# Optimization experiments

Measured on AMD Instinct MI355X. Metric: run time of the kernel, lower is better.

## Reference

```python
import jax, jax.numpy as jnp
import numpy as np

B, L = 2048, 64          # sentence pairs, leaves per balanced binary tree
V, IN, M, HID, NC = 50000, 300, 150, 50, 5


def setup_inputs() -> dict:
    key = jax.random.key(0)
    ks = jax.random.split(key, 16)
    lin = lambda k, fi, fo: jax.random.normal(k, (fi, fo), jnp.float32) / np.sqrt(fi).astype(np.float32)
    bias = lambda k, fo: jax.random.normal(k, (fo,), jnp.float32) * 0.01
    return {
        "ltokens": jax.random.randint(ks[0], (B, L), 0, V, dtype=jnp.int32),
        "rtokens": jax.random.randint(ks[1], (B, L), 0, V, dtype=jnp.int32),
        "emb":   jax.random.normal(ks[2], (V, IN), jnp.float32),
        "Wioux": lin(ks[3], IN, 3 * M), "bioux": bias(ks[4], 3 * M),
        "Wiouh": lin(ks[5], M, 3 * M), "biouh": bias(ks[6], 3 * M),
        "Wfx":   lin(ks[7], IN, M),    "bfx":   bias(ks[8], M),
        "Wfh":   lin(ks[9], M, M),     "bfh":   bias(ks[10], M),
        "Wh":    lin(ks[11], 2 * M, HID), "bh": bias(ks[12], HID),
        "Wp":    lin(ks[13], HID, NC),    "bp": bias(ks[14], NC),
    }


def _split_iou(iou, m):
    return iou[..., :m], iou[..., m:2 * m], iou[..., 2 * m:]


def _encode(tokens, emb, Wioux, bioux, Wiouh, biouh, Wfh, bfh):
    m = Wfh.shape[0]
    x = emb[tokens]                                   # [B, L, IN]
    # Leaves: child_h = child_c = 0, so iouh contributes only its bias and fc = 0.
    iou = x @ Wioux + bioux + biouh                   # [B, L, 3M]
    i, o, u = _split_iou(iou, m)
    c = jax.nn.sigmoid(i) * jnp.tanh(u)
    h = jax.nn.sigmoid(o) * jnp.tanh(c)
    # Internal nodes level by level (inputs=None branch of node_forward).
    while h.shape[1] > 1:
        Bq, n, _ = h.shape
        ch = h.reshape(Bq, n // 2, 2, m)              # children h
        cc = c.reshape(Bq, n // 2, 2, m)              # children c
        iou = ch.sum(axis=2) @ Wiouh + biouh          # child-sum
        i, o, u = _split_iou(iou, m)
        f = jax.nn.sigmoid(ch @ Wfh + bfh)            # per-child forget gate
        c = jax.nn.sigmoid(i) * jnp.tanh(u) + (f * cc).sum(axis=2)
        h = jax.nn.sigmoid(o) * jnp.tanh(c)
    # ROOT in the original just passes its single child's state through.
    return h[:, 0]                                    # [B, M]


def reference(ltokens, rtokens, emb, Wioux, bioux, Wiouh, biouh, Wfx, bfx, Wfh, bfh, Wh, bh, Wp, bp):
    lh = _encode(ltokens, emb, Wioux, bioux, Wiouh, biouh, Wfh, bfh)
    rh = _encode(rtokens, emb, Wioux, bioux, Wiouh, biouh, Wfh, bfh)
    vec = jnp.concatenate([lh * rh, jnp.abs(lh - rh)], axis=-1)   # [B, 2M]
    mid = jax.nn.sigmoid(vec @ Wh + bh)
    return jax.nn.log_softmax(mid @ Wp + bp, axis=-1)             # [B, NC]
```

## Files before the change

### kernel.cpp

```cpp
#include <hip/hip_runtime.h>
#include <hip/hip_bf16.h>
#include <math.h>

constexpr int B_   = 2048;
constexpr int L_   = 64;
constexpr int V_   = 50000;
constexpr int IN_  = 300;
constexpr int M_   = 150;
constexpr int HID_ = 50;
constexpr int NC_  = 5;

constexpr int KP_  = 160;
constexpr int GN_  = 608;
constexpr int GNT_ = 19;
constexpr int GKC_ = 5;
constexpr int GCH_ = GN_ * 32;
constexpr int GQS_ = GN_ * 8;
constexpr int LEAF_N  = 480;
constexpr int LEAF_NT = 15;
constexpr int LEAF_KC = 10;
constexpr int LEAF_CH = LEAF_N * 32;
constexpr int LEAF_QS = LEAF_N * 8;

typedef float f32x4  __attribute__((ext_vector_type(4)));
typedef short bf16x8 __attribute__((ext_vector_type(8)));
typedef short short4v __attribute__((ext_vector_type(4)));

__device__ __forceinline__ float rcp_f(float x) { return __builtin_amdgcn_rcpf(x); }
__device__ __forceinline__ float sgm(float x)   { return rcp_f(1.0f + __expf(-x)); }
__device__ __forceinline__ float tanh_f(float x){ return 1.0f - 2.0f * rcp_f(1.0f + __expf(2.0f * x)); }

__device__ __forceinline__ short f2bs(float f) {
    union { __hip_bfloat16 h; short s; } u; u.h = __float2bfloat16(f); return u.s;
}
__device__ __forceinline__ float bs2f(short s) {
    union { short s; __hip_bfloat16 h; } u; u.s = s; return __bfloat162float(u.h);
}

__device__ __forceinline__ void gl_lds16(const short* g, short* l) {
    __builtin_amdgcn_global_load_lds(
        (const __attribute__((address_space(1))) unsigned int*)g,
        (__attribute__((address_space(3))) unsigned int*)l, 16, 0, 0);
}

__global__ __launch_bounds__(256) void prep_kernel(
    const float* __restrict__ Wioux, const float* __restrict__ Wiouh,
    const float* __restrict__ Wfh, short* __restrict__ Bg, short* __restrict__ Bx)
{
    const int tid = blockIdx.x * blockDim.x + threadIdx.x;
    const int nthr = gridDim.x * blockDim.x;
    const int tot1 = GKC_ * GCH_;
    for (int idx = tid; idx < tot1; idx += nthr) {
        const int kc = idx / GCH_;
        int rem = idx % GCH_;
        const int q = rem / GQS_; rem %= GQS_;
        const int n = rem / 8, j = rem % 8;
        const int k = kc * 32 + q * 8 + j;
        const int m = n >> 2, g = n & 3;
        float v = 0.0f;
        if (k < M_ && m < M_)
            v = (g < 3) ? Wiouh[k * 450 + g * 150 + m] : Wfh[k * M_ + m];
        Bg[idx] = f2bs(v);
    }
    const int tot2 = LEAF_KC * LEAF_CH;
    for (int idx = tid; idx < tot2; idx += nthr) {
        const int kc = idx / LEAF_CH;
        int rem = idx % LEAF_CH;
        const int q = rem / LEAF_QS; rem %= LEAF_QS;
        const int n = rem / 8, j = rem % 8;
        const int k = kc * 32 + q * 8 + j;
        float v = (k < IN_ && n < 450) ? Wioux[k * 450 + n] : 0.0f;
        Bx[idx] = f2bs(v);
    }
}

__global__ __launch_bounds__(512) void leaf_gemm(
    const float* __restrict__ emb, const short* __restrict__ Bx,
    const float* __restrict__ bioux, const float* __restrict__ biouh,
    short* __restrict__ LeafH, short* __restrict__ LeafC)
{
    __shared__ __align__(16) char smem[LEAF_CH * 2 + 64 * 64];
    short* Bs = (short*)smem;
    short* As = (short*)(smem + LEAF_CH * 2);
    float* Es = (float*)smem;

    const int t = threadIdx.x;
    const int row0 = blockIdx.x * 64;
    const int w = t >> 6, lane = t & 63;
    const int mt = w & 3, nt0 = (w >> 2) * LEAF_NT;
    const int lr = lane & 15, quad = lane >> 4;

    f32x4 acc[LEAF_NT];
    #pragma unroll
    for (int i = 0; i < LEAF_NT; i++) { acc[i][0] = 0; acc[i][1] = 0; acc[i][2] = 0; acc[i][3] = 0; }

    const int arow = t >> 3, apart = t & 7;
    const int av = row0 + arow;
    const int aq = apart >> 1, aj = (apart & 1) * 4;

    for (int kc = 0; kc < LEAF_KC; kc++) {
        const short* bsrc = Bx + (size_t)kc * LEAF_CH;
        #pragma unroll
        for (int i = 0; i < 3; i++)
            gl_lds16(bsrc + (i * 512 + t) * 8, Bs + (i * 512 + (t & ~63)) * 8);
        if (t < 384)
            gl_lds16(bsrc + (1536 + t) * 8, Bs + (1536 + (t & ~63)) * 8);
        {
            const int k0 = kc * 32 + apart * 4;
            float4 x = make_float4(0.f, 0.f, 0.f, 0.f);
            if (av < V_ && k0 < IN_) x = *(const float4*)&emb[(size_t)av * IN_ + k0];
            short4v s;
            s[0] = f2bs(x.x); s[1] = f2bs(x.y); s[2] = f2bs(x.z); s[3] = f2bs(x.w);
            *(short4v*)&As[aq * 512 + arow * 8 + aj] = s;
        }
        __syncthreads();
        bf16x8 a = *(const bf16x8*)&As[quad * 512 + (mt * 16 + lr) * 8];
        #pragma unroll
        for (int i = 0; i < LEAF_NT; i++) {
            bf16x8 b = *(const bf16x8*)&Bs[quad * LEAF_QS + ((nt0 + i) * 16 + lr) * 8];
            acc[i] = __builtin_amdgcn_mfma_f32_16x16x32_bf16(a, b, acc[i], 0, 0, 0);
        }
        __syncthreads();
    }

    for (int mc = 0; mc < 4; mc++) {
        if (mt == mc) {
            #pragma unroll
            for (int i = 0; i < LEAF_NT; i++) {
                const int col = (nt0 + i) * 16 + lr;
                #pragma unroll
                for (int r = 0; r < 4; r++) Es[(quad * 4 + r) * LEAF_N + col] = acc[i][r];
            }
        }
        __syncthreads();
        for (int p = t; p < 16 * KP_; p += 512) {
            const int rl = p / KP_, n = p % KP_;
            const int v = row0 + mc * 16 + rl;
            if (v < V_) {
                if (n < M_) {
                    const float i_ = Es[rl * LEAF_N + n]       + bioux[n]       + biouh[n];
                    const float o_ = Es[rl * LEAF_N + n + 150] + bioux[n + 150] + biouh[n + 150];
                    const float u_ = Es[rl * LEAF_N + n + 300] + bioux[n + 300] + biouh[n + 300];
                    const float c = sgm(i_) * tanh_f(u_);
                    const float h = sgm(o_) * tanh_f(c);
                    LeafH[(size_t)v * KP_ + n] = f2bs(h);
                    LeafC[(size_t)v * KP_ + n] = f2bs(c);
                } else {
                    LeafH[(size_t)v * KP_ + n] = 0;
                    LeafC[(size_t)v * KP_ + n] = 0;
                }
            }
        }
        __syncthreads();
    }
}

__global__ __launch_bounds__(512) void leafGF_gemm(
    const short* __restrict__ LeafH, const short* __restrict__ LeafC,
    const short* __restrict__ Bg, const float* __restrict__ bfh,
    short* __restrict__ LeafE)
{
    __shared__ __align__(16) char smem[GCH_ * 2 + 4096 + KP_ * 64 * 2 + 600];
    short* Bs   = (short*)smem;
    short* As   = (short*)(smem + GCH_ * 2);
    short* CinS = (short*)(smem + GCH_ * 2 + 4096);
    float* bfs  = (float*)(smem + GCH_ * 2 + 4096 + KP_ * 64 * 2);
    short* Os   = Bs;

    const int t = threadIdx.x;
    const int v0 = blockIdx.x * 64;
    const int w = t >> 6, lane = t & 63;
    const int mt = w & 3, nt0 = (w >> 2) * GNT_;
    const int lr = lane & 15, quad = lane >> 4;
    const int c = lane & 15;

    if (t < 150) bfs[t] = bfh[t];
    const short* csrc = LeafC + (size_t)v0 * KP_;
    #pragma unroll
    for (int i = 0; i < 2; i++)
        gl_lds16(csrc + (i * 512 + t) * 8, CinS + (i * 512 + (t & ~63)) * 8);
    if (t < 256)
        gl_lds16(csrc + (1024 + t) * 8, CinS + (1024 + (t & ~63)) * 8);

    f32x4 acc[GNT_];
    #pragma unroll
    for (int i = 0; i < GNT_; i++) { acc[i][0] = 0; acc[i][1] = 0; acc[i][2] = 0; acc[i][3] = 0; }

    const int arow = t & 63, apart = t >> 6;
    const size_t srow = (size_t)((v0 + arow < V_) ? (v0 + arow) : 0);
    const short* asrc = LeafH + srow * KP_ + apart * 8;

    for (int kc = 0; kc < GKC_; kc++) {
        const short* bsrc = Bg + (size_t)kc * GCH_;
        #pragma unroll
        for (int i = 0; i < 4; i++)
            gl_lds16(bsrc + (i * 512 + t) * 8, Bs + (i * 512 + (t & ~63)) * 8);
        if (t < 384)
            gl_lds16(bsrc + (2048 + t) * 8, Bs + (2048 + (t & ~63)) * 8);
        if (t < 256)
            gl_lds16(asrc + kc * 32, As + (t & ~63) * 8);
        __syncthreads();
        bf16x8 a = *(const bf16x8*)&As[quad * 512 + (mt * 16 + lr) * 8];
        #pragma unroll
        for (int i = 0; i < GNT_; i++) {
            bf16x8 b = *(const bf16x8*)&Bs[quad * GQS_ + ((nt0 + i) * 16 + lr) * 8];
            acc[i] = __builtin_amdgcn_mfma_f32_16x16x32_bf16(a, b, acc[i], 0, 0, 0);
        }
        __syncthreads();
    }

    for (int ph = 0; ph < 2; ph++) {
        if ((mt >> 1) == ph) {
            const int rbase = 16 * (mt & 1) + 4 * quad;
            #pragma unroll
            for (int i = 0; i < GNT_; i++) {
                const int col = (nt0 + i) * 16 + c;
                const int m = col >> 2, g = col & 3;
                #pragma unroll
                for (int r = 0; r < 4; r++) {
                    short ov;
                    if (g == 3) {
                        if (m < M_) {
                            const float cc = bs2f(CinS[(32 * ph + rbase + r) * KP_ + m]);
                            ov = f2bs(sgm(acc[i][r] + bfs[m]) * cc);
                        } else ov = 0;
                    } else ov = f2bs(acc[i][r]);
                    Os[(rbase + r) * GN_ + col] = ov;
                }
            }
        }
        __syncthreads();
        const int vb = v0 + 32 * ph;
        const int4* os4 = (const int4*)Os;
        for (int u = t; u < 2432; u += 512) {
            const int row = u / 76;
            if (vb + row < V_)
                ((int4*)(LeafE + (size_t)(vb + row) * GN_))[u - row * 76] = os4[u];
        }
        __syncthreads();
    }
}

__device__ __forceinline__ void level_epilogue(
    const f32x4* acc, int mt, int nt0, int lane,
    const short* CinS, const float* bias_s, short* Hs, short* Cs)
{
    const int q = lane >> 4, c = lane & 15, g = c & 3, lb = lane & ~3;
    #pragma unroll
    for (int i = 0; i < GNT_; i++) {
        const int col = (nt0 + i) * 16 + c;
        const int m = col >> 2;
        const float vA = acc[i][0] + acc[i][1];
        const float vB = acc[i][2] + acc[i][3];
        const float iA = __shfl(vA, lb), oA = __shfl(vA, lb + 1), uA = __shfl(vA, lb + 2);
        const float iB = __shfl(vB, lb), oB = __shfl(vB, lb + 1), uB = __shfl(vB, lb + 2);
        const float fA0 = __shfl(acc[i][0], lb + 3), fA1 = __shfl(acc[i][1], lb + 3);
        const float fB0 = __shfl(acc[i][2], lb + 3), fB1 = __shfl(acc[i][3], lb + 3);
        if (g < 2 && m < M_) {
            const float iv = g ? iB : iA, ov = g ? oB : oA, uv = g ? uB : uA;
            const float fl = g ? fB0 : fA0, fr = g ? fB1 : fA1;
            const int node = 8 * mt + 2 * q + g;
            const int ch = 16 * mt + 4 * q + 2 * g;
            const float cl = bs2f(CinS[ch * KP_ + m]);
            const float cr = bs2f(CinS[(ch + 1) * KP_ + m]);
            const float bf = bias_s[450 + m];
            const float cv = sgm(iv + bias_s[m]) * tanh_f(uv + bias_s[m + 300])
                           + sgm(fl + bf) * cl + sgm(fr + bf) * cr;
            const float hv = sgm(ov + bias_s[m + 150]) * tanh_f(cv);
            Hs[node * KP_ + m] = f2bs(hv);
            Cs[node * KP_ + m] = f2bs(cv);
        }
    }
}

__global__ __launch_bounds__(512) void level1_fused(
    const int* __restrict__ ltok, const int* __restrict__ rtok,
    const short* __restrict__ LeafE, const short* __restrict__ Bg,
    const float* __restrict__ biouh, const float* __restrict__ bfh,
    short* __restrict__ Hout, short* __restrict__ Cout)
{
    __shared__ __align__(16) char smem[GCH_ * 2 + 20480 + 20480 + 2400 + 512];
    short* Bs     = (short*)smem;
    short* AsF    = (short*)(smem + GCH_ * 2);
    short* CinS   = (short*)(smem + GCH_ * 2 + 20480);
    float* bias_s = (float*)(smem + GCH_ * 2 + 40960);
    int*   toks   = (int*)(smem + GCH_ * 2 + 43360);
    short* Hs = Bs;
    short* Cs = Bs + 32 * KP_;

    const int t = threadIdx.x;
    const int out0 = blockIdx.x * 32;
    const int w = t >> 6, lane = t & 63;
    const int mt = w & 3, nt0 = (w >> 2) * GNT_;
    const int lr = lane & 15, quad = lane >> 4;

    if (t < 600) bias_s[t] = (t < 450) ? biouh[t] : bfh[t - 450];
    if (t < 128) {
        const int idx = blockIdx.x * 128 + t;
        toks[t] = (idx < B_ * L_) ? ltok[idx] : rtok[idx - B_ * L_];
    }
    __syncthreads();

    {
        const int row = t >> 3, qs = t & 7;
        const short* el = LeafE + (size_t)toks[2 * row] * GN_;
        const short* er = LeafE + (size_t)toks[2 * row + 1] * GN_;
        #pragma unroll
        for (int s = 0; s < 5; s++) {
            const int Q = qs + 8 * s;
            short4v hq = {0, 0, 0, 0}, cq = {0, 0, 0, 0};
            if (Q < 38) {
                union { int4 v[2]; short s16[16]; } ue, ur;
                ue.v[0] = *(const int4*)(el + Q * 16);
                ue.v[1] = *(const int4*)(el + Q * 16 + 8);
                ur.v[0] = *(const int4*)(er + Q * 16);
                ur.v[1] = *(const int4*)(er + Q * 16 + 8);
                #pragma unroll
                for (int jj = 0; jj < 4; jj++) {
                    const int m = 4 * Q + jj;
                    if (m < M_) {
                        const float i_ = bs2f(ue.s16[4 * jj])     + bs2f(ur.s16[4 * jj])     + bias_s[m];
                        const float o_ = bs2f(ue.s16[4 * jj + 1]) + bs2f(ur.s16[4 * jj + 1]) + bias_s[m + 150];
                        const float u_ = bs2f(ue.s16[4 * jj + 2]) + bs2f(ur.s16[4 * jj + 2]) + bias_s[m + 300];
                        const float fc = bs2f(ue.s16[4 * jj + 3]) + bs2f(ur.s16[4 * jj + 3]);
                        const float cv = sgm(i_) * tanh_f(u_) + fc;
                        const float hv = sgm(o_) * tanh_f(cv);
                        hq[jj] = f2bs(hv); cq[jj] = f2bs(cv);
                    }
                }
            }
            const int m0 = 4 * Q;
            const int kc = m0 >> 5, q = (m0 >> 3) & 3, j0 = m0 & 7;
            *(short4v*)&AsF[(kc * 4 + q) * 512 + row * 8 + j0] = hq;
            *(short4v*)&CinS[row * KP_ + m0] = cq;
        }
    }

    f32x4 acc[GNT_];
    #pragma unroll
    for (int i = 0; i < GNT_; i++) { acc[i][0] = 0; acc[i][1] = 0; acc[i][2] = 0; acc[i][3] = 0; }

    for (int kc = 0; kc < GKC_; kc++) {
        const short* bsrc = Bg + (size_t)kc * GCH_;
        #pragma unroll
        for (int i = 0; i < 4; i++)
            gl_lds16(bsrc + (i * 512 + t) * 8, Bs + (i * 512 + (t & ~63)) * 8);
        if (t < 384)
            gl_lds16(bsrc + (2048 + t) * 8, Bs + (2048 + (t & ~63)) * 8);
        __syncthreads();
        bf16x8 a = *(const bf16x8*)&AsF[kc * 2048 + quad * 512 + (mt * 16 + lr) * 8];
        #pragma unroll
        for (int i = 0; i < GNT_; i++) {
            bf16x8 b = *(const bf16x8*)&Bs[quad * GQS_ + ((nt0 + i) * 16 + lr) * 8];
            acc[i] = __builtin_amdgcn_mfma_f32_16x16x32_bf16(a, b, acc[i], 0, 0, 0);
        }
        __syncthreads();
    }

    if (t < 320) { const int node = t / 10, mm = 150 + t % 10;
                   Hs[node * KP_ + mm] = 0; Cs[node * KP_ + mm] = 0; }
    level_epilogue(acc, mt, nt0, lane, CinS, bias_s, Hs, Cs);
    __syncthreads();
    int4* Hg = (int4*)(Hout + (size_t)out0 * KP_);
    int4* Cg = (int4*)(Cout + (size_t)out0 * KP_);
    const int4* hs4 = (const int4*)Hs;
    const int4* cs4 = (const int4*)Cs;
    for (int u = t; u < 1280; u += 512) {
        if (u < 640) Hg[u] = hs4[u]; else Cg[u - 640] = cs4[u - 640];
    }
}

__global__ __launch_bounds__(512) void level_gemm(
    const short* __restrict__ Hin, const short* __restrict__ Cin,
    const short* __restrict__ Bg,
    const float* __restrict__ biouh, const float* __restrict__ bfh,
    short* __restrict__ Hout, short* __restrict__ Cout)
{
    __shared__ __align__(16) char smem[GCH_ * 2 + 4096 + 20480 + 2400];
    short* Bs     = (short*)smem;
    short* As     = (short*)(smem + GCH_ * 2);
    short* CinS   = (short*)(smem + GCH_ * 2 + 4096);
    float* bias_s = (float*)(smem + GCH_ * 2 + 4096 + 20480);
    short* Hs = Bs;
    short* Cs = Bs + 32 * KP_;

    const int t = threadIdx.x;
    const int row0 = blockIdx.x * 64, out0 = blockIdx.x * 32;
    const int w = t >> 6, lane = t & 63;
    const int mt = w & 3, nt0 = (w >> 2) * GNT_;
    const int lr = lane & 15, quad = lane >> 4;

    if (t < 600) bias_s[t] = (t < 450) ? biouh[t] : bfh[t - 450];
    const short* csrc = Cin + (size_t)row0 * KP_;
    #pragma unroll
    for (int i = 0; i < 2; i++)
        gl_lds16(csrc + (i * 512 + t) * 8, CinS + (i * 512 + (t & ~63)) * 8);
    if (t < 256)
        gl_lds16(csrc + (1024 + t) * 8, CinS + (1024 + (t & ~63)) * 8);

    f32x4 acc[GNT_];
    #pragma unroll
    for (int i = 0; i < GNT_; i++) { acc[i][0] = 0; acc[i][1] = 0; acc[i][2] = 0; acc[i][3] = 0; }

    const short* asrc = Hin + (size_t)(row0 + (t & 63)) * KP_ + (t >> 6) * 8;

    for (int kc = 0; kc < GKC_; kc++) {
        const short* bsrc = Bg + (size_t)kc * GCH_;
        #pragma unroll
        for (int i = 0; i < 4; i++)
            gl_lds16(bsrc + (i * 512 + t) * 8, Bs + (i * 512 + (t & ~63)) * 8);
        if (t < 384)
            gl_lds16(bsrc + (2048 + t) * 8, Bs + (2048 + (t & ~63)) * 8);
        if (t < 256)
            gl_lds16(asrc + kc * 32, As + (t & ~63) * 8);
        __syncthreads();
        bf16x8 a = *(const bf16x8*)&As[quad * 512 + (mt * 16 + lr) * 8];
        #pragma unroll
        for (int i = 0; i < GNT_; i++) {
            bf16x8 b = *(const bf16x8*)&Bs[quad * GQS_ + ((nt0 + i) * 16 + lr) * 8];
            acc[i] = __builtin_amdgcn_mfma_f32_16x16x32_bf16(a, b, acc[i], 0, 0, 0);
        }
        __syncthreads();
    }

    if (t < 320) { const int node = t / 10, mm = 150 + t % 10;
                   Hs[node * KP_ + mm] = 0; Cs[node * KP_ + mm] = 0; }
    level_epilogue(acc, mt, nt0, lane, CinS, bias_s, Hs, Cs);
    __syncthreads();
    int4* Hg = (int4*)(Hout + (size_t)out0 * KP_);
    int4* Cg = (int4*)(Cout + (size_t)out0 * KP_);
    const int4* hs4 = (const int4*)Hs;
    const int4* cs4 = (const int4*)Cs;
    for (int u = t; u < 1280; u += 512) {
        if (u < 640) Hg[u] = hs4[u]; else Cg[u - 640] = cs4[u - 640];
    }
}

__global__ __launch_bounds__(64) void head_kernel(
    const short* __restrict__ RootH,
    const float* __restrict__ Wh, const float* __restrict__ bh,
    const float* __restrict__ Wp, const float* __restrict__ bp,
    float* __restrict__ out)
{
    __shared__ float vec[2 * M_];
    __shared__ float mid[HID_];
    __shared__ float lg[NC_];
    __shared__ float lse;

    const int b = blockIdx.x;
    const int t = threadIdx.x;
    const short* lh = RootH + (size_t)b * KP_;
    const short* rh = RootH + (size_t)(B_ + b) * KP_;

    for (int i = t; i < M_; i += 64) {
        const float a = bs2f(lh[i]), c = bs2f(rh[i]);
        vec[i]      = a * c;
        vec[M_ + i] = fabsf(a - c);
    }
    __syncthreads();

    for (int j = t; j < HID_; j += 64) {
        float acc = bh[j];
        for (int k = 0; k < 2 * M_; k++) acc += vec[k] * Wh[k * HID_ + j];
        mid[j] = sgm(acc);
    }
    __syncthreads();

    if (t < NC_) {
        float acc = bp[t];
        for (int k = 0; k < HID_; k++) acc += mid[k] * Wp[k * NC_ + t];
        lg[t] = acc;
    }
    __syncthreads();

    if (t == 0) {
        float mx = lg[0];
        for (int i = 1; i < NC_; i++) mx = fmaxf(mx, lg[i]);
        float s = 0.0f;
        for (int i = 0; i < NC_; i++) s += expf(lg[i] - mx);
        lse = mx + logf(s);
    }
    __syncthreads();

    if (t < NC_) out[b * NC_ + t] = lg[t] - lse;
}

extern "C" void kernel_launch(void* const* d_in, const int* in_sizes, int n_in,
                              void* d_out, int out_size, void* d_ws, size_t ws_size,
                              hipStream_t stream)
{
    const int*   ltok  = (const int*)d_in[0];
    const int*   rtok  = (const int*)d_in[1];
    const float* emb   = (const float*)d_in[2];
    const float* Wioux = (const float*)d_in[3];
    const float* bioux = (const float*)d_in[4];
    const float* Wiouh = (const float*)d_in[5];
    const float* biouh = (const float*)d_in[6];
    const float* Wfh   = (const float*)d_in[9];
    const float* bfh   = (const float*)d_in[10];
    const float* Wh    = (const float*)d_in[11];
    const float* bh    = (const float*)d_in[12];
    const float* Wp    = (const float*)d_in[13];
    const float* bp    = (const float*)d_in[14];
    float* out = (float*)d_out;

    char* ws = (char*)d_ws;
    size_t off = 0;
    auto carve = [&](size_t bytes) { char* p = ws + off; off += (bytes + 255) & ~(size_t)255; return p; };
    short* Bg    = (short*)carve((size_t)GKC_ * GCH_ * 2);
    short* Bx    = (short*)carve((size_t)LEAF_KC * LEAF_CH * 2);
    short* LeafH = (short*)carve((size_t)V_ * KP_ * 2);
    short* LeafC = (short*)carve((size_t)V_ * KP_ * 2);
    short* LeafE = (short*)carve((size_t)V_ * GN_ * 2);
    short* HA    = (short*)carve((size_t)65536 * KP_ * 2);
    short* CA    = (short*)carve((size_t)65536 * KP_ * 2);
    short* HB    = (short*)carve((size_t)32768 * KP_ * 2);
    short* CB    = (short*)carve((size_t)32768 * KP_ * 2);

    hipLaunchKernelGGL(prep_kernel, dim3(128), dim3(256), 0, stream, Wioux, Wiouh, Wfh, Bg, Bx);
    hipLaunchKernelGGL(leaf_gemm, dim3((V_ + 63) / 64), dim3(512), 0, stream,
                       emb, Bx, bioux, biouh, LeafH, LeafC);
    hipLaunchKernelGGL(leafGF_gemm, dim3((V_ + 63) / 64), dim3(512), 0, stream,
                       LeafH, LeafC, Bg, bfh, LeafE);
    hipLaunchKernelGGL(level1_fused, dim3(2048), dim3(512), 0, stream,
                       ltok, rtok, LeafE, Bg, biouh, bfh, HA, CA);
    hipLaunchKernelGGL(level_gemm, dim3(1024), dim3(512), 0, stream,
                       HA, CA, Bg, biouh, bfh, HB, CB);
    hipLaunchKernelGGL(level_gemm, dim3(512), dim3(512), 0, stream,
                       HB, CB, Bg, biouh, bfh, HA, CA);
    hipLaunchKernelGGL(level_gemm, dim3(256), dim3(512), 0, stream,
                       HA, CA, Bg, biouh, bfh, HB, CB);
    hipLaunchKernelGGL(level_gemm, dim3(128), dim3(512), 0, stream,
                       HB, CB, Bg, biouh, bfh, HA, CA);
    hipLaunchKernelGGL(head_kernel, dim3(B_), dim3(64), 0, stream, HA, Wh, bh, Wp, bp, out);
}
```

Baseline: 537.2 us.

## Fuse leaf embedding GEMM with leaf gate GEMM, keep leaf state in LDS

Merges the leaf_gemm and leafGF_gemm kernels into a single leafE_gemm kernel. Leaf h and c for a 64-row vocabulary tile stay in shared memory and feed the Wiouh/Wfh GEMM directly, so the LeafH/LeafC global round trip and one launch go away. level1_fused now prefetches the first B chunk before its token gather and reads tokens straight from global memory. Shared memory per block grows to about 81 KB, which may lower occupancy, and the c buffer stride becomes 152.

Result: no change. 543.8 us (+1.2%).

```diff
diff --git a/kernel.cpp b/kernel.cpp
--- a/kernel.cpp
+++ b/kernel.cpp
@@ -11,6 +11,7 @@
 constexpr int NC_  = 5;
 
 constexpr int KP_  = 160;
+constexpr int CS_  = 152;
 constexpr int GN_  = 608;
 constexpr int GNT_ = 19;
 constexpr int GKC_ = 5;
@@ -74,28 +75,36 @@
     }
 }
 
-__global__ __launch_bounds__(512) void leaf_gemm(
+__global__ __launch_bounds__(512) void leafE_gemm(
     const float* __restrict__ emb, const short* __restrict__ Bx,
+    const short* __restrict__ Bg,
     const float* __restrict__ bioux, const float* __restrict__ biouh,
-    short* __restrict__ LeafH, short* __restrict__ LeafC)
-{
-    __shared__ __align__(16) char smem[LEAF_CH * 2 + 64 * 64];
-    short* Bs = (short*)smem;
-    short* As = (short*)(smem + LEAF_CH * 2);
-    float* Es = (float*)smem;
+    const float* __restrict__ bfh, short* __restrict__ LeafE)
+{
+    __shared__ __align__(16) char smem[81248];
+    short* Bs     = (short*)smem;
+    short* AsF    = (short*)(smem + 38912);
+    short* As     = AsF;
+    short* CinS   = (short*)(smem + 59392);
+    float* bias_s = (float*)(smem + 78848);
+    float* Es     = (float*)smem;
+    short* Os     = Bs;
 
     const int t = threadIdx.x;
-    const int row0 = blockIdx.x * 64;
+    const int v0 = blockIdx.x * 64;
     const int w = t >> 6, lane = t & 63;
-    const int mt = w & 3, nt0 = (w >> 2) * LEAF_NT;
+    const int mt = w & 3;
     const int lr = lane & 15, quad = lane >> 4;
 
-    f32x4 acc[LEAF_NT];
+    if (t < 600) bias_s[t] = (t < 450) ? (bioux[t] + biouh[t]) : bfh[t - 450];
+
+    const int nt1 = (w >> 2) * LEAF_NT;
+    f32x4 acc[GNT_];
     #pragma unroll
     for (int i = 0; i < LEAF_NT; i++) { acc[i][0] = 0; acc[i][1] = 0; acc[i][2] = 0; acc[i][3] = 0; }
 
     const int arow = t >> 3, apart = t & 7;
-    const int av = row0 + arow;
+    const int av = v0 + arow;
     const int aq = apart >> 1, aj = (apart & 1) * 4;
 
     for (int kc = 0; kc < LEAF_KC; kc++) {
@@ -117,7 +126,7 @@
         bf16x8 a = *(const bf16x8*)&As[quad * 512 + (mt * 16 + lr) * 8];
         #pragma unroll
         for (int i = 0; i < LEAF_NT; i++) {
-            bf16x8 b = *(const bf16x8*)&Bs[quad * LEAF_QS + ((nt0 + i) * 16 + lr) * 8];
+            bf16x8 b = *(const bf16x8*)&Bs[quad * LEAF_QS + ((nt1 + i) * 16 + lr) * 8];
             acc[i] = __builtin_amdgcn_mfma_f32_16x16x32_bf16(a, b, acc[i], 0, 0, 0);
         }
         __syncthreads();
@@ -127,68 +136,41 @@
         if (mt == mc) {
             #pragma unroll
             for (int i = 0; i < LEAF_NT; i++) {
-                const int col = (nt0 + i) * 16 + lr;
+                const int col = (nt1 + i) * 16 + lr;
                 #pragma unroll
                 for (int r = 0; r < 4; r++) Es[(quad * 4 + r) * LEAF_N + col] = acc[i][r];
             }
         }
         __syncthreads();
-        for (int p = t; p < 16 * KP_; p += 512) {
-            const int rl = p / KP_, n = p % KP_;
-            const int v = row0 + mc * 16 + rl;
-            if (v < V_) {
-                if (n < M_) {
-                    const float i_ = Es[rl * LEAF_N + n]       + bioux[n]       + biouh[n];
-                    const float o_ = Es[rl * LEAF_N + n + 150] + bioux[n + 150] + biouh[n + 150];
-                    const float u_ = Es[rl * LEAF_N + n + 300] + bioux[n + 300] + biouh[n + 300];
-                    const float c = sgm(i_) * tanh_f(u_);
-                    const float h = sgm(o_) * tanh_f(c);
-                    LeafH[(size_t)v * KP_ + n] = f2bs(h);
-                    LeafC[(size_t)v * KP_ + n] = f2bs(c);
-                } else {
-                    LeafH[(size_t)v * KP_ + n] = 0;
-                    LeafC[(size_t)v * KP_ + n] = 0;
+        for (int p = t; p < 640; p += 512) {
+            const int rl = p / 40, Q = p % 40;
+            const int m0 = 4 * Q;
+            short4v hq = {0, 0, 0, 0}, cq = {0, 0, 0, 0};
+            if (Q < 38) {
+                #pragma unroll
+                for (int jj = 0; jj < 4; jj++) {
+                    const int m = m0 + jj;
+                    if (m < M_) {
+                        const float i_ = Es[rl * LEAF_N + m]       + bias_s[m];
+                        const float o_ = Es[rl * LEAF_N + m + 150] + bias_s[m + 150];
+                        const float u_ = Es[rl * LEAF_N + m + 300] + bias_s[m + 300];
+                        const float c = sgm(i_) * tanh_f(u_);
+                        const float h = sgm(o_) * tanh_f(c);
+                        hq[jj] = f2bs(h); cq[jj] = f2bs(c);
+                    }
                 }
             }
-        }
-        __syncthreads();
-    }
-}
-
-__global__ __launch_bounds__(512) void leafGF_gemm(
-    const short* __restrict__ LeafH, const short* __restrict__ LeafC,
-    const short* __restrict__ Bg, const float* __restrict__ bfh,
-    short* __restrict__ LeafE)
-{
-    __shared__ __align__(16) char smem[GCH_ * 2 + 4096 + KP_ * 64 * 2 + 600];
-    short* Bs   = (short*)smem;
-    short* As   = (short*)(smem + GCH_ * 2);
-    short* CinS = (short*)(smem + GCH_ * 2 + 4096);
-    float* bfs  = (float*)(smem + GCH_ * 2 + 4096 + KP_ * 64 * 2);
-    short* Os   = Bs;
-
-    const int t = threadIdx.x;
-    const int v0 = blockIdx.x * 64;
-    const int w = t >> 6, lane = t & 63;
-    const int mt = w & 3, nt0 = (w >> 2) * GNT_;
-    const int lr = lane & 15, quad = lane >> 4;
-    const int c = lane & 15;
-
-    if (t < 150) bfs[t] = bfh[t];
-    const short* csrc = LeafC + (size_t)v0 * KP_;
-    #pragma unroll
-    for (int i = 0; i < 2; i++)
-        gl_lds16(csrc + (i * 512 + t) * 8, CinS + (i * 512 + (t & ~63)) * 8);
-    if (t < 256)
-        gl_lds16(csrc + (1024 + t) * 8, CinS + (1024 + (t & ~63)) * 8);
-
-    f32x4 acc[GNT_];
+            const int row = mc * 16 + rl;
+            const int kc = m0 >> 5, q = (m0 >> 3) & 3, j0 = m0 & 7;
+            *(short4v*)&AsF[(kc * 4 + q) * 512 + row * 8 + j0] = hq;
+            if (m0 < M_) *(short4v*)&CinS[row * CS_ + m0] = cq;
+        }
+        __syncthreads();
+    }
+
+    const int nt2 = (w >> 2) * GNT_;
     #pragma unroll
     for (int i = 0; i < GNT_; i++) { acc[i][0] = 0; acc[i][1] = 0; acc[i][2] = 0; acc[i][3] = 0; }
-
-    const int arow = t & 63, apart = t >> 6;
-    const size_t srow = (size_t)((v0 + arow < V_) ? (v0 + arow) : 0);
-    const short* asrc = LeafH + srow * KP_ + apart * 8;
 
     for (int kc = 0; kc < GKC_; kc++) {
         const short* bsrc = Bg + (size_t)kc * GCH_;
@@ -197,32 +179,31 @@
             gl_lds16(bsrc + (i * 512 + t) * 8, Bs + (i * 512 + (t & ~63)) * 8);
         if (t < 384)
             gl_lds16(bsrc + (2048 + t) * 8, Bs + (2048 + (t & ~63)) * 8);
-        if (t < 256)
-            gl_lds16(asrc + kc * 32, As + (t & ~63) * 8);
-        __syncthreads();
-        bf16x8 a = *(const bf16x8*)&As[quad * 512 + (mt * 16 + lr) * 8];
+        __syncthreads();
+        bf16x8 a = *(const bf16x8*)&AsF[kc * 2048 + quad * 512 + (mt * 16 + lr) * 8];
         #pragma unroll
         for (int i = 0; i < GNT_; i++) {
-            bf16x8 b = *(const bf16x8*)&Bs[quad * GQS_ + ((nt0 + i) * 16 + lr) * 8];
+            bf16x8 b = *(const bf16x8*)&Bs[quad * GQS_ + ((nt2 + i) * 16 + lr) * 8];
             acc[i] = __builtin_amdgcn_mfma_f32_16x16x32_bf16(a, b, acc[i], 0, 0, 0);
         }
         __syncthreads();
     }
 
+    const int c = lane & 15;
     for (int ph = 0; ph < 2; ph++) {
         if ((mt >> 1) == ph) {
             const int rbase = 16 * (mt & 1) + 4 * quad;
             #pragma unroll
             for (int i = 0; i < GNT_; i++) {
-                const int col = (nt0 + i) * 16 + c;
+                const int col = (nt2 + i) * 16 + c;
                 const int m = col >> 2, g = col & 3;
                 #pragma unroll
                 for (int r = 0; r < 4; r++) {
                     short ov;
                     if (g == 3) {
                         if (m < M_) {
-                            const float cc = bs2f(CinS[(32 * ph + rbase + r) * KP_ + m]);
-                            ov = f2bs(sgm(acc[i][r] + bfs[m]) * cc);
+                            const float cc = bs2f(CinS[(32 * ph + rbase + r) * CS_ + m]);
+                            ov = f2bs(sgm(acc[i][r] + bias_s[450 + m]) * cc);
                         } else ov = 0;
                     } else ov = f2bs(acc[i][r]);
                     Os[(rbase + r) * GN_ + col] = ov;
@@ -243,7 +224,7 @@
 
 __device__ __forceinline__ void level_epilogue(
     const f32x4* acc, int mt, int nt0, int lane,
-    const short* CinS, const float* bias_s, short* Hs, short* Cs)
+    const short* CinS, int cstride, const float* bias_s, short* Hs, short* Cs)
 {
     const int q = lane >> 4, c = lane & 15, g = c & 3, lb = lane & ~3;
     #pragma unroll
@@ -261,8 +242,8 @@
             const float fl = g ? fB0 : fA0, fr = g ? fB1 : fA1;
             const int node = 8 * mt + 2 * q + g;
             const int ch = 16 * mt + 4 * q + 2 * g;
-            const float cl = bs2f(CinS[ch * KP_ + m]);
-            const float cr = bs2f(CinS[(ch + 1) * KP_ + m]);
+            const float cl = bs2f(CinS[ch * cstride + m]);
+            const float cr = bs2f(CinS[(ch + 1) * cstride + m]);
             const float bf = bias_s[450 + m];
             const float cv = sgm(iv + bias_s[m]) * tanh_f(uv + bias_s[m + 300])
                            + sgm(fl + bf) * cl + sgm(fr + bf) * cr;
@@ -279,12 +260,11 @@
     const float* __restrict__ biouh, const float* __restrict__ bfh,
     short* __restrict__ Hout, short* __restrict__ Cout)
 {
-    __shared__ __align__(16) char smem[GCH_ * 2 + 20480 + 20480 + 2400 + 512];
+    __shared__ __align__(16) char smem[81248];
     short* Bs     = (short*)smem;
-    short* AsF    = (short*)(smem + GCH_ * 2);
-    short* CinS   = (short*)(smem + GCH_ * 2 + 20480);
-    float* bias_s = (float*)(smem + GCH_ * 2 + 40960);
-    int*   toks   = (int*)(smem + GCH_ * 2 + 43360);
+    short* AsF    = (short*)(smem + 38912);
+    short* CinS   = (short*)(smem + 59392);
+    float* bias_s = (float*)(smem + 78848);
     short* Hs = Bs;
     short* Cs = Bs + 32 * KP_;
 
@@ -294,17 +274,25 @@
     const int mt = w & 3, nt0 = (w >> 2) * GNT_;
     const int lr = lane & 15, quad = lane >> 4;
 
+    {
+        const short* bsrc = Bg;
+        #pragma unroll
+        for (int i = 0; i < 4; i++)
+            gl_lds16(bsrc + (i * 512 + t) * 8, Bs + (i * 512 + (t & ~63)) * 8);
+        if (t < 384)
+            gl_lds16(bsrc + (2048 + t) * 8, Bs + (2048 + (t & ~63)) * 8);
+    }
     if (t < 600) bias_s[t] = (t < 450) ? biouh[t] : bfh[t - 450];
-    if (t < 128) {
-        const int idx = blockIdx.x * 128 + t;
-        toks[t] = (idx < B_ * L_) ? ltok[idx] : rtok[idx - B_ * L_];
-    }
     __syncthreads();
 
     {
         const int row = t >> 3, qs = t & 7;
-        const short* el = LeafE + (size_t)toks[2 * row] * GN_;
-        const short* er = LeafE + (size_t)toks[2 * row + 1] * GN_;
+        const int half = B_ * L_;
+        const int gidx = blockIdx.x * 128 + 2 * row;
+        const int tl = (gidx < half) ? ltok[gidx] : rtok[gidx - half];
+        const int tr = (gidx + 1 < half) ? ltok[gidx + 1] : rtok[gidx + 1 - half];
+        const short* el = LeafE + (size_t)tl * GN_;
+        const short* er = LeafE + (size_t)tr * GN_;
         #pragma unroll
         for (int s = 0; s < 5; s++) {
             const int Q = qs + 8 * s;
@@ -332,7 +320,7 @@
             const int m0 = 4 * Q;
             const int kc = m0 >> 5, q = (m0 >> 3) & 3, j0 = m0 & 7;
             *(short4v*)&AsF[(kc * 4 + q) * 512 + row * 8 + j0] = hq;
-            *(short4v*)&CinS[row * KP_ + m0] = cq;
+            if (m0 < M_) *(short4v*)&CinS[row * CS_ + m0] = cq;
         }
     }
 
@@ -341,12 +329,14 @@
     for (int i = 0; i < GNT_; i++) { acc[i][0] = 0; acc[i][1] = 0; acc[i][2] = 0; acc[i][3] = 0; }
 
     for (int kc = 0; kc < GKC_; kc++) {
-        const short* bsrc = Bg + (size_t)kc * GCH_;
-        #pragma unroll
-        for (int i = 0; i < 4; i++)
-            gl_lds16(bsrc + (i * 512 + t) * 8, Bs + (i * 512 + (t & ~63)) * 8);
-        if (t < 384)
-            gl_lds16(bsrc + (2048 + t) * 8, Bs + (2048 + (t & ~63)) * 8);
+        if (kc > 0) {
+            const short* bsrc = Bg + (size_t)kc * GCH_;
+            #pragma unroll
+            for (int i = 0; i < 4; i++)
+                gl_lds16(bsrc + (i * 512 + t) * 8, Bs + (i * 512 + (t & ~63)) * 8);
+            if (t < 384)
+                gl_lds16(bsrc + (2048 + t) * 8, Bs + (2048 + (t & ~63)) * 8);
+        }
         __syncthreads();
         bf16x8 a = *(const bf16x8*)&AsF[kc * 2048 + quad * 512 + (mt * 16 + lr) * 8];
         #pragma unroll
@@ -359,7 +349,7 @@
 
     if (t < 320) { const int node = t / 10, mm = 150 + t % 10;
                    Hs[node * KP_ + mm] = 0; Cs[node * KP_ + mm] = 0; }
-    level_epilogue(acc, mt, nt0, lane, CinS, bias_s, Hs, Cs);
+    level_epilogue(acc, mt, nt0, lane, CinS, CS_, bias_s, Hs, Cs);
     __syncthreads();
     int4* Hg = (int4*)(Hout + (size_t)out0 * KP_);
     int4* Cg = (int4*)(Cout + (size_t)out0 * KP_);
@@ -425,7 +415,7 @@
 
     if (t < 320) { const int node = t / 10, mm = 150 + t % 10;
                    Hs[node * KP_ + mm] = 0; Cs[node * KP_ + mm] = 0; }
-    level_epilogue(acc, mt, nt0, lane, CinS, bias_s, Hs, Cs);
+    level_epilogue(acc, mt, nt0, lane, CinS, KP_, bias_s, Hs, Cs);
     __syncthreads();
     int4* Hg = (int4*)(Hout + (size_t)out0 * KP_);
     int4* Cg = (int4*)(Cout + (size_t)out0 * KP_);
@@ -509,8 +499,6 @@
     auto carve = [&](size_t bytes) { char* p = ws + off; off += (bytes + 255) & ~(size_t)255; return p; };
     short* Bg    = (short*)carve((size_t)GKC_ * GCH_ * 2);
     short* Bx    = (short*)carve((size_t)LEAF_KC * LEAF_CH * 2);
-    short* LeafH = (short*)carve((size_t)V_ * KP_ * 2);
-    short* LeafC = (short*)carve((size_t)V_ * KP_ * 2);
     short* LeafE = (short*)carve((size_t)V_ * GN_ * 2);
     short* HA    = (short*)carve((size_t)65536 * KP_ * 2);
     short* CA    = (short*)carve((size_t)65536 * KP_ * 2);
@@ -518,10 +506,8 @@
     short* CB    = (short*)carve((size_t)32768 * KP_ * 2);
 
     hipLaunchKernelGGL(prep_kernel, dim3(128), dim3(256), 0, stream, Wioux, Wiouh, Wfh, Bg, Bx);
-    hipLaunchKernelGGL(leaf_gemm, dim3((V_ + 63) / 64), dim3(512), 0, stream,
-                       emb, Bx, bioux, biouh, LeafH, LeafC);
-    hipLaunchKernelGGL(leafGF_gemm, dim3((V_ + 63) / 64), dim3(512), 0, stream,
-                       LeafH, LeafC, Bg, bfh, LeafE);
+    hipLaunchKernelGGL(leafE_gemm, dim3((V_ + 63) / 64), dim3(512), 0, stream,
+                       emb, Bx, Bg, bioux, biouh, bfh, LeafE);
     hipLaunchKernelGGL(level1_fused, dim3(2048), dim3(512), 0, stream,
                        ltok, rtok, LeafE, Bg, biouh, bfh, HA, CA);
     hipLaunchKernelGGL(level_gemm, dim3(1024), dim3(512), 0, stream,
```
